# Kernel optimization log

Hardware: AMD Instinct MI355X
Metric: run time of the kernel (lower is better)

## Reference

```python
import jax, jax.numpy as jnp
import numpy as np

BETA = 0.8
THR = 1.0  # snntorch Leaky default threshold


def _heaviside(x):
    return (x > 0).astype(x.dtype)


def setup_inputs() -> dict:
    key = jax.random.key(0)
    ks = jax.random.split(key, 8)
    B, T, F, H, L, O = 256, 512, 8, 256, 4, 8
    x = jax.random.normal(ks[0], (B, T, F), dtype=jnp.float32)
    hidden_states = jnp.zeros((B, T, L, H), dtype=jnp.float32)
    prev_obs = jnp.zeros((B, T, F), dtype=jnp.float32)
    readout_states = jnp.zeros((B, T, O), dtype=jnp.float32)
    # fc1: Linear(8, H)
    W1 = jax.random.normal(ks[1], (F, H), dtype=jnp.float32) / np.sqrt(F)
    b1 = jnp.zeros((H,), dtype=jnp.float32)
    # hidden linears: L-1 of [H,H]; final linear [H,O]
    Wh = jax.random.normal(ks[2], (L - 1, H, H), dtype=jnp.float32) / np.sqrt(H)
    bh = jnp.zeros((L - 1, H), dtype=jnp.float32)
    Wout = jax.random.normal(ks[3], (H, O), dtype=jnp.float32) / np.sqrt(H)
    bout = jnp.zeros((O,), dtype=jnp.float32)
    return {"x": x, "hidden_states": hidden_states, "prev_obs": prev_obs,
            "readout_states": readout_states, "W1": W1, "b1": b1,
            "Wh": Wh, "bh": bh, "Wout": Wout, "bout": bout}


def reference(x, hidden_states, prev_obs, readout_states, W1, b1, Wh, bh, Wout, bout):
    # x: [B,T,F]; hidden_states: [B,T,L,H]; readout_states: [B,T,O]
    L = Wh.shape[0] + 1
    mem0 = hidden_states[:, 0]          # [B,L,H]
    ro0 = readout_states[:, 0]          # [B,O]
    # fc1 applied to all timesteps at once (as in the original)
    all_cur = jnp.einsum('btf,fh->bth', x, W1) + b1  # [B,T,H]

    def step(carry, cur_t):
        mem, ro = carry                 # mem: [B,L,H], ro: [B,O]
        cur = cur_t                     # [B,H]
        for i in range(L):
            m = mem[:, i]
            # snntorch Leaky (reset_mechanism='subtract'):
            # reset computed from previous mem, detached
            reset = _heaviside(m - THR)
            m = BETA * m + cur - reset * THR
            spk = _heaviside(m - THR)
            mem = mem.at[:, i].set(m)
            if i < L - 1:
                cur = spk @ Wh[i] + bh[i]
            else:
                cur = spk @ Wout + bout  # [B,O]
        # readout Leaky with reset_mechanism='none'
        ro = BETA * ro + cur
        return (mem, ro), (ro, mem)

    (_, _), (ros, mems) = jax.lax.scan(step, (mem0, ro0), jnp.swapaxes(all_cur, 0, 1))
    outputs = jnp.swapaxes(ros, 0, 1)            # [B,T,O]
    new_hidden_states = jnp.swapaxes(mems, 0, 1)  # [B,T,L,H]
    new_prev_obs = x
    new_readout_states = outputs
    return outputs, new_hidden_states, new_prev_obs, new_readout_states
```

## Files before the change

### kernel.cpp

```cpp
#include <hip/hip_runtime.h>

#define BB   256
#define TT   512
#define FF   8
#define HH   256
#define LL   4
#define OO   8
#define BETA 0.8f
#define THRV 1.0f

#define OFF_OUT  0
#define OFF_HID  (BB*TT*OO)
#define OFF_PREV (OFF_HID + (size_t)BB*TT*LL*HH)
#define OFF_RO   (OFF_PREV + BB*TT*FF)

typedef float nf4 __attribute__((ext_vector_type(4)));

__device__ __forceinline__ float scan_sum(const int* lst, int n, const float* __restrict__ Wb)
{
    float cc = 0.f;
    int j = 0;
    if (n >= 8) {
        int4 e0 = *(const int4*)(lst);
        int4 e1 = *(const int4*)(lst + 4);
        float w0 = Wb[e0.x], w1 = Wb[e0.y], w2 = Wb[e0.z], w3 = Wb[e0.w];
        float w4 = Wb[e1.x], w5 = Wb[e1.y], w6 = Wb[e1.z], w7 = Wb[e1.w];
        j = 8;
        while (j + 7 < n) {
            int4 f0 = *(const int4*)(lst + j);
            int4 f1 = *(const int4*)(lst + j + 4);
            float v0 = Wb[f0.x], v1 = Wb[f0.y], v2 = Wb[f0.z], v3 = Wb[f0.w];
            float v4 = Wb[f1.x], v5 = Wb[f1.y], v6 = Wb[f1.z], v7 = Wb[f1.w];
            cc += ((w0 + w1) + (w2 + w3)) + ((w4 + w5) + (w6 + w7));
            w0 = v0; w1 = v1; w2 = v2; w3 = v3;
            w4 = v4; w5 = v5; w6 = v6; w7 = v7;
            j += 8;
        }
        cc += ((w0 + w1) + (w2 + w3)) + ((w4 + w5) + (w6 + w7));
    }
    if (j < n) {
        int4 e0 = *(const int4*)(lst + j);
        int4 e1 = *(const int4*)(lst + j + 4);
        float w0 = Wb[e0.x], w1 = Wb[e0.y], w2 = Wb[e0.z], w3 = Wb[e0.w];
        float w4 = Wb[e1.x], w5 = Wb[e1.y], w6 = Wb[e1.z], w7 = Wb[e1.w];
        cc += (j + 0 < n ? w0 : 0.f) + (j + 1 < n ? w1 : 0.f)
            + (j + 2 < n ? w2 : 0.f) + (j + 3 < n ? w3 : 0.f)
            + (j + 4 < n ? w4 : 0.f) + (j + 5 < n ? w5 : 0.f)
            + (j + 6 < n ? w6 : 0.f) + (j + 7 < n ? w7 : 0.f);
    }
    return cc;
}

#define UPDATE_PUBLISH(mreg, li, cval)                                          \
    {                                                                           \
        float reset_ = ((mreg) > THRV) ? THRV : 0.f;                            \
        (mreg) = BETA * (mreg) + (cval) - reset_;                               \
        int spk_ = ((mreg) > THRV) ? 1 : 0;                                     \
        __builtin_nontemporal_store((mreg), hrow + (li) * HH + h);              \
        unsigned long long bm_ = __ballot(spk_);                                \
        int base_ = 0;                                                          \
        if (lane == 0) base_ = atomicAdd(&s_total[li], __popcll(bm_));          \
        base_ = __shfl(base_, 0);                                               \
        if (spk_)                                                               \
            s_list[li][base_ + __popcll(bm_ & ((1ull << lane) - 1ull))] = h << 8;\
    }

__launch_bounds__(320, 1)
__global__ void snn_kernel(const float* __restrict__ x,
                           const float* __restrict__ hidden_in,
                           const float* __restrict__ readout_in,
                           const float* __restrict__ W1,
                           const float* __restrict__ b1,
                           const float* __restrict__ Wh,
                           const float* __restrict__ bh,
                           const float* __restrict__ Wout,
                           const float* __restrict__ bout,
                           float* __restrict__ out)
{
    __shared__ int                s_list[3][264];
    __shared__ int                s_total[3];
    __shared__ unsigned long long s_mask3[4];

    const int tid  = threadIdx.x;
    const int b    = blockIdx.x;
    const int lane = tid & 63;
    const int wave = tid >> 6;
    const int h    = tid & (HH - 1);

    for (int i = tid; i < 3 * 264; i += 320) ((int*)s_list)[i] = 0;
    if (tid < 3) s_total[tid] = 0;
    if (tid < 4) s_mask3[tid] = 0ull;

    {
        const nf4* xs = (const nf4*)(x + (size_t)b * TT * FF);
        nf4*       po = (nf4*)(out + OFF_PREV + (size_t)b * TT * FF);
        for (int i = tid; i < (TT * FF) / 4; i += 320)
            __builtin_nontemporal_store(xs[i], po + i);
    }

    float m0 = 0, m1 = 0, m2 = 0, m3 = 0;
    float w1c[FF];
    float b1c = 0, bhc0 = 0, bhc1 = 0, bhc2 = 0;
    if (tid < 256) {
        const size_t hb = (size_t)b * TT * LL * HH;
        m0 = hidden_in[hb + 0 * HH + h];
        m1 = hidden_in[hb + 1 * HH + h];
        m2 = hidden_in[hb + 2 * HH + h];
        m3 = hidden_in[hb + 3 * HH + h];
        #pragma unroll
        for (int f = 0; f < FF; ++f) w1c[f] = W1[f * HH + h];
        b1c  = b1[h];
        bhc0 = bh[0 * HH + h]; bhc1 = bh[1 * HH + h]; bhc2 = bh[2 * HH + h];
    }

    const int o8  = lane & 7;
    const int seg = lane >> 3;
    float ro = 0.f, boutc = 0.f;
    if (wave == 4 && lane < 8) {
        ro    = readout_in[(size_t)b * TT * OO + lane];
        boutc = bout[lane];
    }

    const float* xb  = x + (size_t)b * TT * FF;
    const float* Wb0 = Wh + h;
    const float* Wb1 = Wh + 1 * HH * HH + h;
    const float* Wb2 = Wh + 2 * HH * HH + h;
    float* hid_out = out + OFF_HID + (size_t)b * TT * LL * HH;
    float* out_o   = out + OFF_OUT + (size_t)b * TT * OO;
    float* out_r   = out + OFF_RO  + (size_t)b * TT * OO;

    nf4 xv0 = {0, 0, 0, 0}, xv1 = {0, 0, 0, 0};
    if (tid < 256) { xv0 = ((const nf4*)xb)[0]; xv1 = ((const nf4*)xb)[1]; }

    __syncthreads();

    #pragma unroll 1
    for (int t = 0; t < TT; ++t) {
        float* hrow = hid_out + (size_t)t * LL * HH;

        if (tid < 256) {
            float c = b1c + xv0.x * w1c[0] + xv0.y * w1c[1] + xv0.z * w1c[2] + xv0.w * w1c[3]
                          + xv1.x * w1c[4] + xv1.y * w1c[5] + xv1.z * w1c[6] + xv1.w * w1c[7];
            UPDATE_PUBLISH(m0, 0, c);
        } else if (tid == 256) {
            s_total[2] = 0;
        }
        __syncthreads();

        if (tid < 256) {
            const int tn = (t + 1 < TT) ? t + 1 : t;
            xv0 = ((const nf4*)(xb + tn * FF))[0];
            xv1 = ((const nf4*)(xb + tn * FF))[1];
            float c = bhc0 + scan_sum(s_list[0], s_total[0], Wb0);
            UPDATE_PUBLISH(m1, 1, c);
        } else if (t > 0) {
            unsigned sm = ((const unsigned*)s_mask3)[seg];
            float acc = 0.f;
            while (sm) {
                int r = __builtin_ctz(sm);
                sm &= sm - 1;
                acc += Wout[((seg << 5) + r) * OO + o8];
            }
            acc += __shfl_xor(acc, 8);
            acc += __shfl_xor(acc, 16);
            acc += __shfl_xor(acc, 32);
            if (lane < 8) {
                ro = BETA * ro + (acc + boutc);
                __builtin_nontemporal_store(ro, out_o + (t - 1) * OO + lane);
                __builtin_nontemporal_store(ro, out_r + (t - 1) * OO + lane);
            }
        }
        __syncthreads();

        if (tid < 256) {
            float c = bhc1 + scan_sum(s_list[1], s_total[1], Wb1);
            UPDATE_PUBLISH(m2, 2, c);
        } else if (tid == 256) {
            s_total[0] = 0;
        }
        __syncthreads();

        if (tid < 256) {
            float c = bhc2 + scan_sum(s_list[2], s_total[2], Wb2);
            float reset_ = (m3 > THRV) ? THRV : 0.f;
            m3 = BETA * m3 + c - reset_;
            int spk_ = (m3 > THRV) ? 1 : 0;
            __builtin_nontemporal_store(m3, hrow + 3 * HH + h);
            unsigned long long bm_ = __ballot(spk_);
            if (lane == 0) s_mask3[wave] = bm_;
        } else if (tid == 256) {
            s_total[1] = 0;
        }
        __syncthreads();
    }

    if (wave == 4) {
        unsigned sm = ((const unsigned*)s_mask3)[seg];
        float acc = 0.f;
        while (sm) {
            int r = __builtin_ctz(sm);
            sm &= sm - 1;
            acc += Wout[((seg << 5) + r) * OO + o8];
        }
        acc += __shfl_xor(acc, 8);
        acc += __shfl_xor(acc, 16);
        acc += __shfl_xor(acc, 32);
        if (lane < 8) {
            ro = BETA * ro + (acc + boutc);
            __builtin_nontemporal_store(ro, out_o + (TT - 1) * OO + lane);
            __builtin_nontemporal_store(ro, out_r + (TT - 1) * OO + lane);
        }
    }
}

extern "C" void kernel_launch(void* const* d_in, const int* in_sizes, int n_in,
                              void* d_out, int out_size, void* d_ws, size_t ws_size,
                              hipStream_t stream) {
    const float* x       = (const float*)d_in[0];
    const float* hidden  = (const float*)d_in[1];
    const float* readout = (const float*)d_in[3];
    const float* W1      = (const float*)d_in[4];
    const float* b1      = (const float*)d_in[5];
    const float* Wh      = (const float*)d_in[6];
    const float* bh      = (const float*)d_in[7];
    const float* Wout    = (const float*)d_in[8];
    const float* bout    = (const float*)d_in[9];
    float* out = (float*)d_out;

    snn_kernel<<<dim3(BB), dim3(320), 0, stream>>>(
        x, hidden, readout, W1, b1, Wh, bh, Wout, bout, out);
}
```

Baseline: 1.899 ms.

## Fold next-step layer-0 update into layer-3 phase and chunk spike-list sums

Moves the layer-0 membrane update for step t+1 into the same barrier phase as the layer-3 update of step t, cutting one __syncthreads per timestep (four down to three). It also replaces the 8-wide pipelined gather sum over the spike list with 32-element chunks that are gathered and then reduced as a tree, which raises memory-level parallelism. The chunked version always reads a full 32-entry list prefix and adds register pressure. The list arrays are shrunk to 256 entries and aligned to 16 bytes. The s_total[0] reset and list reuse ordering now rely on the shifted phase layout.

```diff
diff --git a/kernel.cpp b/kernel.cpp
--- a/kernel.cpp
+++ b/kernel.cpp
@@ -16,47 +16,70 @@
 
 typedef float nf4 __attribute__((ext_vector_type(4)));
 
-__device__ __forceinline__ float scan_sum(const int* lst, int n, const float* __restrict__ Wb)
+__device__ __forceinline__ float tree32_masked(const float* W, int base, int n) {
+    float t[32];
+    #pragma unroll
+    for (int q = 0; q < 32; ++q) t[q] = (base + q < n) ? W[q] : 0.f;
+    #pragma unroll
+    for (int s = 16; s > 0; s >>= 1)
+        #pragma unroll
+        for (int q = 0; q < s; ++q) t[q] += t[q + s];
+    return t[0];
+}
+
+__device__ __forceinline__ float tree32(const float* W) {
+    float t[32];
+    #pragma unroll
+    for (int q = 0; q < 32; ++q) t[q] = W[q];
+    #pragma unroll
+    for (int s = 16; s > 0; s >>= 1)
+        #pragma unroll
+        for (int q = 0; q < s; ++q) t[q] += t[q + s];
+    return t[0];
+}
+
+__device__ __forceinline__ float scan_chunks(const int* lst, int n, const float* __restrict__ Wb)
 {
-    float cc = 0.f;
-    int j = 0;
-    if (n >= 8) {
-        int4 e0 = *(const int4*)(lst);
-        int4 e1 = *(const int4*)(lst + 4);
-        float w0 = Wb[e0.x], w1 = Wb[e0.y], w2 = Wb[e0.z], w3 = Wb[e0.w];
-        float w4 = Wb[e1.x], w5 = Wb[e1.y], w6 = Wb[e1.z], w7 = Wb[e1.w];
-        j = 8;
-        while (j + 7 < n) {
-            int4 f0 = *(const int4*)(lst + j);
-            int4 f1 = *(const int4*)(lst + j + 4);
-            float v0 = Wb[f0.x], v1 = Wb[f0.y], v2 = Wb[f0.z], v3 = Wb[f0.w];
-            float v4 = Wb[f1.x], v5 = Wb[f1.y], v6 = Wb[f1.z], v7 = Wb[f1.w];
-            cc += ((w0 + w1) + (w2 + w3)) + ((w4 + w5) + (w6 + w7));
-            w0 = v0; w1 = v1; w2 = v2; w3 = v3;
-            w4 = v4; w5 = v5; w6 = v6; w7 = v7;
-            j += 8;
-        }
-        cc += ((w0 + w1) + (w2 + w3)) + ((w4 + w5) + (w6 + w7));
-    }
-    if (j < n) {
-        int4 e0 = *(const int4*)(lst + j);
-        int4 e1 = *(const int4*)(lst + j + 4);
-        float w0 = Wb[e0.x], w1 = Wb[e0.y], w2 = Wb[e0.z], w3 = Wb[e0.w];
-        float w4 = Wb[e1.x], w5 = Wb[e1.y], w6 = Wb[e1.z], w7 = Wb[e1.w];
-        cc += (j + 0 < n ? w0 : 0.f) + (j + 1 < n ? w1 : 0.f)
-            + (j + 2 < n ? w2 : 0.f) + (j + 3 < n ? w3 : 0.f)
-            + (j + 4 < n ? w4 : 0.f) + (j + 5 < n ? w5 : 0.f)
-            + (j + 6 < n ? w6 : 0.f) + (j + 7 < n ? w7 : 0.f);
-    }
-    return cc;
-}
-
-#define UPDATE_PUBLISH(mreg, li, cval)                                          \
+    int4 La[8];
+    #pragma unroll
+    for (int q = 0; q < 8; ++q) La[q] = ((const int4*)lst)[q];
+    if (n <= 0) return 0.f;
+    float Wa[32];
+    #pragma unroll
+    for (int q = 0; q < 8; ++q) {
+        Wa[4*q+0] = Wb[La[q].x]; Wa[4*q+1] = Wb[La[q].y];
+        Wa[4*q+2] = Wb[La[q].z]; Wa[4*q+3] = Wb[La[q].w];
+    }
+    if (n <= 32) return tree32_masked(Wa, 0, n);
+
+    float acc = 0.f;
+    int base = 0;
+    const int nch = (n + 31) >> 5;
+    #pragma unroll 1
+    for (int c = 1; c < nch; ++c) {
+        int4 Lb[8];
+        #pragma unroll
+        for (int q = 0; q < 8; ++q) Lb[q] = ((const int4*)(lst + 32 * c))[q];
+        float Wn[32];
+        #pragma unroll
+        for (int q = 0; q < 8; ++q) {
+            Wn[4*q+0] = Wb[Lb[q].x]; Wn[4*q+1] = Wb[Lb[q].y];
+            Wn[4*q+2] = Wb[Lb[q].z]; Wn[4*q+3] = Wb[Lb[q].w];
+        }
+        acc += tree32(Wa);
+        #pragma unroll
+        for (int q = 0; q < 32; ++q) Wa[q] = Wn[q];
+        base += 32;
+    }
+    return acc + tree32_masked(Wa, base, n);
+}
+
+#define UPDATE_PUBLISH(mreg, li, cval, rowptr)                                  \
     {                                                                           \
         float reset_ = ((mreg) > THRV) ? THRV : 0.f;                            \
         (mreg) = BETA * (mreg) + (cval) - reset_;                               \
         int spk_ = ((mreg) > THRV) ? 1 : 0;                                     \
-        __builtin_nontemporal_store((mreg), hrow + (li) * HH + h);              \
+        __builtin_nontemporal_store((mreg), (rowptr) + h);                      \
         unsigned long long bm_ = __ballot(spk_);                                \
         int base_ = 0;                                                          \
         if (lane == 0) base_ = atomicAdd(&s_total[li], __popcll(bm_));          \
@@ -77,7 +100,7 @@
                            const float* __restrict__ bout,
                            float* __restrict__ out)
 {
-    __shared__ int                s_list[3][264];
+    __shared__ __align__(16) int s_list[3][256];
     __shared__ int                s_total[3];
     __shared__ unsigned long long s_mask3[4];
 
@@ -87,7 +110,7 @@
     const int wave = tid >> 6;
     const int h    = tid & (HH - 1);
 
-    for (int i = tid; i < 3 * 264; i += 320) ((int*)s_list)[i] = 0;
+    for (int i = tid; i < 3 * 256; i += 320) ((int*)s_list)[i] = 0;
     if (tid < 3) s_total[tid] = 0;
     if (tid < 4) s_mask3[tid] = 0ull;
 
@@ -130,60 +153,72 @@
     float* out_r   = out + OFF_RO  + (size_t)b * TT * OO;
 
     nf4 xv0 = {0, 0, 0, 0}, xv1 = {0, 0, 0, 0};
-    if (tid < 256) { xv0 = ((const nf4*)xb)[0]; xv1 = ((const nf4*)xb)[1]; }
-
+
+    __syncthreads();
+
+    if (tid < 256) {
+        xv0 = ((const nf4*)xb)[0];
+        xv1 = ((const nf4*)xb)[1];
+        float c = b1c + xv0.x * w1c[0] + xv0.y * w1c[1] + xv0.z * w1c[2] + xv0.w * w1c[3]
+                      + xv1.x * w1c[4] + xv1.y * w1c[5] + xv1.z * w1c[6] + xv1.w * w1c[7];
+        UPDATE_PUBLISH(m0, 0, c, hid_out + 0);
+    }
     __syncthreads();
 
     #pragma unroll 1
     for (int t = 0; t < TT; ++t) {
         float* hrow = hid_out + (size_t)t * LL * HH;
-
-        if (tid < 256) {
-            float c = b1c + xv0.x * w1c[0] + xv0.y * w1c[1] + xv0.z * w1c[2] + xv0.w * w1c[3]
-                          + xv1.x * w1c[4] + xv1.y * w1c[5] + xv1.z * w1c[6] + xv1.w * w1c[7];
-            UPDATE_PUBLISH(m0, 0, c);
-        } else if (tid == 256) {
-            s_total[2] = 0;
-        }
-        __syncthreads();
 
         if (tid < 256) {
             const int tn = (t + 1 < TT) ? t + 1 : t;
             xv0 = ((const nf4*)(xb + tn * FF))[0];
             xv1 = ((const nf4*)(xb + tn * FF))[1];
-            float c = bhc0 + scan_sum(s_list[0], s_total[0], Wb0);
-            UPDATE_PUBLISH(m1, 1, c);
-        } else if (t > 0) {
-            unsigned sm = ((const unsigned*)s_mask3)[seg];
-            float acc = 0.f;
-            while (sm) {
-                int r = __builtin_ctz(sm);
-                sm &= sm - 1;
-                acc += Wout[((seg << 5) + r) * OO + o8];
+            int n0 = s_total[0];
+            float c = bhc0 + scan_chunks(s_list[0], n0, Wb0);
+            UPDATE_PUBLISH(m1, 1, c, hrow + HH);
+        } else {
+            if (tid == 256) s_total[2] = 0;
+            if (t > 0) {
+                unsigned sm = ((const unsigned*)s_mask3)[seg];
+                float acc = 0.f;
+                while (sm) {
+                    int r = __builtin_ctz(sm);
+                    sm &= sm - 1;
+                    acc += Wout[((seg << 5) + r) * OO + o8];
+                }
+                acc += __shfl_xor(acc, 8);
+                acc += __shfl_xor(acc, 16);
+                acc += __shfl_xor(acc, 32);
+                if (lane < 8) {
+                    ro = BETA * ro + (acc + boutc);
+                    __builtin_nontemporal_store(ro, out_o + (t - 1) * OO + lane);
+                    __builtin_nontemporal_store(ro, out_r + (t - 1) * OO + lane);
+                }
             }
-            acc += __shfl_xor(acc, 8);
-            acc += __shfl_xor(acc, 16);
-            acc += __shfl_xor(acc, 32);
-            if (lane < 8) {
-                ro = BETA * ro + (acc + boutc);
-                __builtin_nontemporal_store(ro, out_o + (t - 1) * OO + lane);
-                __builtin_nontemporal_store(ro, out_r + (t - 1) * OO + lane);
-            }
         }
         __syncthreads();
 
         if (tid < 256) {
-            float c = bhc1 + scan_sum(s_list[1], s_total[1], Wb1);
-            UPDATE_PUBLISH(m2, 2, c);
+            int n1 = s_total[1];
+            float c = bhc1 + scan_chunks(s_list[1], n1, Wb1);
+            UPDATE_PUBLISH(m2, 2, c, hrow + 2 * HH);
         } else if (tid == 256) {
             s_total[0] = 0;
         }
         __syncthreads();
 
         if (tid < 256) {
-            float c = bhc2 + scan_sum(s_list[2], s_total[2], Wb2);
+            int n2 = s_total[2];
+            float c2 = bhc2 + scan_chunks(s_list[2], n2, Wb2);
+
+            if (t + 1 < TT) {
+                float c0 = b1c + xv0.x * w1c[0] + xv0.y * w1c[1] + xv0.z * w1c[2] + xv0.w * w1c[3]
+                               + xv1.x * w1c[4] + xv1.y * w1c[5] + xv1.z * w1c[6] + xv1.w * w1c[7];
+                UPDATE_PUBLISH(m0, 0, c0, hrow + LL * HH);
+            }
+
             float reset_ = (m3 > THRV) ? THRV : 0.f;
-            m3 = BETA * m3 + c - reset_;
+            m3 = BETA * m3 + c2 - reset_;
             int spk_ = (m3 > THRV) ? 1 : 0;
             __builtin_nontemporal_store(m3, hrow + 3 * HH + h);
             unsigned long long bm_ = __ballot(spk_);
```

Result: slower. 2.051 ms (+8.0%).
